# Kernel optimization log

Measured on AMD Instinct MI355X. Metric: run time of the kernel, lower is better.

Reference implementation:

```python
import jax, jax.numpy as jnp
import numpy as np

N = 100_000   # num destination nodes (adj rows)
M = 100_000   # num source/neighbor nodes (adj cols)
E = 3_200_000 # num edges (avg degree 32)
D_IN = 128
DIM = 128
LEAKY_ALPHA = 0.2  # tf.nn.leaky_relu default


def setup_inputs() -> dict:
    key = jax.random.key(0)
    ks = jax.random.split(key, 7)
    return {
        "self_embedding": jax.random.normal(ks[0], (N, D_IN), jnp.float32),
        "neigh_embedding": jax.random.normal(ks[1], (M, D_IN), jnp.float32),
        "W": jax.random.normal(ks[2], (D_IN, DIM), jnp.float32) / np.sqrt(D_IN).astype(np.float32),
        "w_self": jax.random.normal(ks[3], (DIM, 1), jnp.float32) * 0.1,
        "w_neigh": jax.random.normal(ks[4], (DIM, 1), jnp.float32) * 0.1,
        "edge_row": jax.random.randint(ks[5], (E,), 0, N, jnp.int32),
        "edge_col": jax.random.randint(ks[6], (E,), 0, M, jnp.int32),
    }


def reference(self_embedding, neigh_embedding, W, w_self, w_neigh, edge_row, edge_col):
    # Dense projections (shared weight, no bias)
    from_all = neigh_embedding @ W    # [M, DIM]
    from_self = self_embedding @ W    # [N, DIM]

    # Per-node attention logits
    self_weight = (from_self @ w_self)[:, 0]   # [N]
    all_weight = (from_all @ w_neigh)[:, 0]    # [M]

    # Per-edge score: leaky_relu(self_weight[row] + all_weight[col])
    scores = jax.nn.leaky_relu(self_weight[edge_row] + all_weight[edge_col],
                               negative_slope=LEAKY_ALPHA)  # [E]

    n = self_embedding.shape[0]
    # Sparse (segment) softmax over each row's edges, numerically stable
    row_max = jax.ops.segment_max(scores, edge_row, num_segments=n)
    row_max = jnp.where(jnp.isfinite(row_max), row_max, 0.0)  # guard empty rows
    e = jnp.exp(scores - row_max[edge_row])
    denom = jax.ops.segment_sum(e, edge_row, num_segments=n)
    denom = jnp.where(denom > 0, denom, 1.0)
    alpha = e / denom[edge_row]  # [E]

    # Sparse-dense matmul: output[i] = sum_j alpha_ij * from_all[j]
    agg = jax.ops.segment_sum(alpha[:, None] * from_all[edge_col], edge_row,
                              num_segments=n)  # [N, DIM]

    # renorm=False path: residual with from_self, then activation
    return jax.nn.relu(from_self + agg)
```

## Files before the change

### kernel.cpp

```cpp
#include <hip/hip_runtime.h>
#include <math.h>

#define DIM 128
#define LEAKY 0.2f
#define CAP 80
#define RPB 128
#define NBMAX 1024
#define PART_CHUNK 4096

typedef __attribute__((ext_vector_type(8))) short short8_t;
typedef __attribute__((ext_vector_type(8))) __bf16 bf16x8;
typedef __attribute__((ext_vector_type(4))) float f32x4;

__device__ __forceinline__ unsigned short f32_to_bf16_bits(float x) {
  unsigned u = __float_as_uint(x);
  u += 0x7fffu + ((u >> 16) & 1u);
  return (unsigned short)(u >> 16);
}

template <typename OT>
__global__ __launch_bounds__(256) void gemm_proj_mfma(
    const float* __restrict__ emb, const float* __restrict__ W,
    const float* __restrict__ wvec, OT* __restrict__ out,
    float* __restrict__ wout, int nrows)
{
  __shared__ unsigned short Wt[128 * 136];
  int t = threadIdx.x;
  int lane = t & 63;
  int wid = t >> 6;

  for (int i = t; i < 4096; i += 256) {
    int k = i >> 5;
    int c4 = (i & 31) << 2;
    float4 w4 = *(const float4*)(W + k * 128 + c4);
    Wt[(c4 + 0) * 136 + k] = f32_to_bf16_bits(w4.x);
    Wt[(c4 + 1) * 136 + k] = f32_to_bf16_bits(w4.y);
    Wt[(c4 + 2) * 136 + k] = f32_to_bf16_bits(w4.z);
    Wt[(c4 + 3) * 136 + k] = f32_to_bf16_bits(w4.w);
  }
  __syncthreads();

  int row0 = blockIdx.x * 128 + wid * 32;
  if (row0 >= nrows) return;

  int lr = lane & 15;
  int lk = lane >> 4;

  bf16x8 a[2][4];
#pragma unroll
  for (int rf = 0; rf < 2; rf++) {
    int row = row0 + rf * 16 + lr;
    row = min(row, nrows - 1);
    const float* src = emb + (size_t)row * DIM;
#pragma unroll
    for (int ks = 0; ks < 4; ks++) {
      int kb = ks * 32 + lk * 8;
      float4 x = *(const float4*)(src + kb);
      float4 y = *(const float4*)(src + kb + 4);
      union { short8_t s; bf16x8 b; } f;
      f.s[0] = (short)f32_to_bf16_bits(x.x); f.s[1] = (short)f32_to_bf16_bits(x.y);
      f.s[2] = (short)f32_to_bf16_bits(x.z); f.s[3] = (short)f32_to_bf16_bits(x.w);
      f.s[4] = (short)f32_to_bf16_bits(y.x); f.s[5] = (short)f32_to_bf16_bits(y.y);
      f.s[6] = (short)f32_to_bf16_bits(y.z); f.s[7] = (short)f32_to_bf16_bits(y.w);
      a[rf][ks] = f.b;
    }
  }

  f32x4 acc[2][8];
#pragma unroll
  for (int rf = 0; rf < 2; rf++)
#pragma unroll
    for (int cf = 0; cf < 8; cf++)
      acc[rf][cf] = (f32x4){0.f, 0.f, 0.f, 0.f};

#pragma unroll
  for (int ks = 0; ks < 4; ks++) {
#pragma unroll
    for (int cf = 0; cf < 8; cf++) {
      bf16x8 wf = *(const bf16x8*)(Wt + (cf * 16 + lr) * 136 + ks * 32 + lk * 8);
      acc[0][cf] = __builtin_amdgcn_mfma_f32_16x16x32_bf16(a[0][ks], wf, acc[0][cf], 0, 0, 0);
      acc[1][cf] = __builtin_amdgcn_mfma_f32_16x16x32_bf16(a[1][ks], wf, acc[1][cf], 0, 0, 0);
    }
  }

#pragma unroll
  for (int rf = 0; rf < 2; rf++) {
    float pp[4] = {0.f, 0.f, 0.f, 0.f};
#pragma unroll
    for (int cf = 0; cf < 8; cf++) {
      float wvv = wvec[cf * 16 + lr];
#pragma unroll
      for (int r = 0; r < 4; r++) pp[r] += acc[rf][cf][r] * wvv;
    }
#pragma unroll
    for (int r = 0; r < 4; r++) {
      pp[r] += __shfl_xor(pp[r], 1);
      pp[r] += __shfl_xor(pp[r], 2);
      pp[r] += __shfl_xor(pp[r], 4);
      pp[r] += __shfl_xor(pp[r], 8);
    }
#pragma unroll
    for (int r = 0; r < 4; r++) {
      int row = row0 + rf * 16 + lk * 4 + r;
      if (row < nrows) {
        if (lr == 0) wout[row] = pp[r];
#pragma unroll
        for (int cf = 0; cf < 8; cf++) {
          int col = cf * 16 + lr;
          if constexpr (sizeof(OT) == 4)
            ((float*)out)[(size_t)row * DIM + col] = acc[rf][cf][r];
          else
            ((unsigned short*)out)[(size_t)row * DIM + col] = f32_to_bf16_bits(acc[rf][cf][r]);
        }
      }
    }
  }
}

__global__ __launch_bounds__(256) void quantize_rows(
    const unsigned short* __restrict__ fa_bf16,
    unsigned char* __restrict__ fa_i8, float* __restrict__ scales, int M)
{
  int wid = threadIdx.x >> 6;
  int lane = threadIdx.x & 63;
  int row = blockIdx.x * 4 + wid;
  if (row >= M) return;
  unsigned u = ((const unsigned*)(fa_bf16 + (size_t)row * DIM))[lane];
  float v0 = __uint_as_float(u << 16);
  float v1 = __uint_as_float(u & 0xffff0000u);
  float m = fmaxf(fabsf(v0), fabsf(v1));
#pragma unroll
  for (int off = 32; off >= 1; off >>= 1) m = fmaxf(m, __shfl_xor(m, off));
  float inv = m > 0.f ? 127.f / m : 0.f;
  int q0 = (int)__builtin_rintf(v0 * inv) + 128;
  int q1 = (int)__builtin_rintf(v1 * inv) + 128;
  ((unsigned short*)(fa_i8 + (size_t)row * DIM))[lane] =
      (unsigned short)((q0 & 0xff) | ((q1 & 0xff) << 8));
  if (lane == 0) scales[row] = m * (1.f / 127.f);
}

__global__ void zero_gcur(int* __restrict__ gcur, int nb)
{
  int i = blockIdx.x * blockDim.x + threadIdx.x;
  if (i < nb) gcur[i] = 0;
}

__global__ __launch_bounds__(256) void partition_edges(
    const int* __restrict__ erow, const int* __restrict__ ecol,
    unsigned* __restrict__ streams, int capB, int* __restrict__ gcur,
    int E, int nb)
{
  __shared__ int cnt[NBMAX];
  __shared__ int base_[NBMAX];
  __shared__ int pos[NBMAX];
  int t = threadIdx.x;
  for (int i = t; i < nb; i += 256) { cnt[i] = 0; pos[i] = 0; }
  __syncthreads();

  int e0 = blockIdx.x * PART_CHUNK + t * 16;
  int rows[16], cols[16];
#pragma unroll
  for (int q = 0; q < 4; q++) {
    int e = e0 + q * 4;
    if (e + 3 < E) {
      *(int4*)(rows + q * 4) = *(const int4*)(erow + e);
      *(int4*)(cols + q * 4) = *(const int4*)(ecol + e);
    } else {
#pragma unroll
      for (int j = 0; j < 4; j++) {
        rows[q * 4 + j] = (e + j < E) ? erow[e + j] : -1;
        cols[q * 4 + j] = (e + j < E) ? ecol[e + j] : 0;
      }
    }
  }
#pragma unroll
  for (int j = 0; j < 16; j++)
    if (rows[j] >= 0) atomicAdd(&cnt[rows[j] >> 7], 1);
  __syncthreads();
  for (int i = t; i < nb; i += 256)
    base_[i] = cnt[i] ? atomicAdd(gcur + i, cnt[i]) : 0;
  __syncthreads();
#pragma unroll
  for (int j = 0; j < 16; j++) {
    if (rows[j] >= 0) {
      int b = rows[j] >> 7;
      int idx = base_[b] + atomicAdd(&pos[b], 1);
      if (idx < capB)
        streams[(size_t)b * capB + idx] =
            (unsigned)cols[j] | ((unsigned)(rows[j] & (RPB - 1)) << 20);
    }
  }
}

__global__ __launch_bounds__(256) void bucket_scatter(
    const unsigned* __restrict__ streams, int capB,
    const int* __restrict__ gcur, int* __restrict__ perm,
    int* __restrict__ deg, int N)
{
  __shared__ __align__(16) unsigned slots[RPB * CAP];
  __shared__ int cnt[RPB];
  int b = blockIdx.x;
  int t = threadIdx.x;
  for (int i = t; i < RPB; i += 256) cnt[i] = 0;
  __syncthreads();

  int n = min(gcur[b], capB);
  const unsigned* s = streams + (size_t)b * capB;
  for (int i = t; i < n; i += 256) {
    unsigned v = s[i];
    int rl = v >> 20;
    int p = atomicAdd(&cnt[rl], 1);
    if (p < CAP) slots[rl * CAP + p] = v & 0xFFFFFu;
  }
  __syncthreads();

  int row0 = b * RPB;
  unsigned* dst = (unsigned*)(perm + (size_t)row0 * CAP);
  for (int i = t; i < RPB * CAP / 4; i += 256)
    *(uint4*)(dst + i * 4) = *(const uint4*)(slots + i * 4);
  for (int i = t; i < RPB; i += 256) {
    int row = row0 + i;
    if (row < N) deg[row] = min(cnt[i], CAP);
  }
}

__global__ __launch_bounds__(256) void aggregate_kernel(
    const unsigned char* __restrict__ fa_i8,
    const float* __restrict__ scales,
    const int* __restrict__ perm, const int* __restrict__ deg_arr,
    const float* __restrict__ sw, const float* __restrict__ aw,
    float* __restrict__ out, int n)
{
  int wid = threadIdx.x >> 6;
  int lane = threadIdx.x & 63;
  int row = blockIdx.x * 4 + wid;
  if (row >= n) return;
  int deg = deg_arr[row];
  size_t base = (size_t)row * CAP;

  int g  = lane >> 3;
  int sl = lane & 7;

  size_t o = (size_t)row * DIM + sl * 16;
  float4 rr0, rr1, rr2, rr3;
  if (g == 0) {
    rr0 = *(const float4*)(out + o);
    rr1 = *(const float4*)(out + o + 4);
    rr2 = *(const float4*)(out + o + 8);
    rr3 = *(const float4*)(out + o + 12);
  }

  float acc[16];
#pragma unroll
  for (int k = 0; k < 16; k++) acc[k] = 0.f;
  float dsum = 0.f, Bl = 0.f;
  float swr = sw[row];

  for (int bb = 0; bb < deg; bb += 64) {
    int nact = min(64, deg - bb);
    int c = 0; float e = 0.f, a = 0.f;
    if (lane < nact) {
      c = perm[base + bb + lane];
      float v = swr + aw[c];
      v = v > 0.f ? v : LEAKY * v;
      e = __expf(v);
      a = e * scales[c];
    }
    dsum += e;

    for (int half = 0; half < 2; half++) {
      if (half * 32 >= nact) break;
#pragma unroll
      for (int jj = 0; jj < 4; jj++) {
        int eidx = half * 32 + (jj << 3) + g;
        float aj = __shfl(a, eidx);
        int   cj = __shfl(c, eidx);
        uint4 u = *(const uint4*)(fa_i8 + (size_t)cj * DIM + sl * 16);
        Bl += aj;
        acc[0]  += aj * (float)( u.x        & 0xffu);
        acc[1]  += aj * (float)((u.x >> 8 ) & 0xffu);
        acc[2]  += aj * (float)((u.x >> 16) & 0xffu);
        acc[3]  += aj * (float)( u.x >> 24);
        acc[4]  += aj * (float)( u.y        & 0xffu);
        acc[5]  += aj * (float)((u.y >> 8 ) & 0xffu);
        acc[6]  += aj * (float)((u.y >> 16) & 0xffu);
        acc[7]  += aj * (float)( u.y >> 24);
        acc[8]  += aj * (float)( u.z        & 0xffu);
        acc[9]  += aj * (float)((u.z >> 8 ) & 0xffu);
        acc[10] += aj * (float)((u.z >> 16) & 0xffu);
        acc[11] += aj * (float)( u.z >> 24);
        acc[12] += aj * (float)( u.w        & 0xffu);
        acc[13] += aj * (float)((u.w >> 8 ) & 0xffu);
        acc[14] += aj * (float)((u.w >> 16) & 0xffu);
        acc[15] += aj * (float)( u.w >> 24);
      }
    }
  }

#pragma unroll
  for (int off = 32; off >= 1; off >>= 1) dsum += __shfl_xor(dsum, off);
  Bl += __shfl_xor(Bl, 8); Bl += __shfl_xor(Bl, 16); Bl += __shfl_xor(Bl, 32);
#pragma unroll
  for (int k = 0; k < 16; k++) {
    acc[k] += __shfl_xor(acc[k], 8);
    acc[k] += __shfl_xor(acc[k], 16);
    acc[k] += __shfl_xor(acc[k], 32);
  }
  float B = -128.f * Bl;
  float inv = dsum > 0.f ? 1.f / dsum : 1.f;

  if (g == 0) {
    float r[16] = {rr0.x, rr0.y, rr0.z, rr0.w, rr1.x, rr1.y, rr1.z, rr1.w,
                   rr2.x, rr2.y, rr2.z, rr2.w, rr3.x, rr3.y, rr3.z, rr3.w};
#pragma unroll
    for (int k = 0; k < 16; k++) {
      float x = r[k] + (acc[k] + B) * inv;
      r[k] = x > 0.f ? x : 0.f;
    }
    *(float4*)(out + o)      = make_float4(r[0],  r[1],  r[2],  r[3]);
    *(float4*)(out + o + 4)  = make_float4(r[4],  r[5],  r[6],  r[7]);
    *(float4*)(out + o + 8)  = make_float4(r[8],  r[9],  r[10], r[11]);
    *(float4*)(out + o + 12) = make_float4(r[12], r[13], r[14], r[15]);
  }
}

extern "C" void kernel_launch(void* const* d_in, const int* in_sizes, int n_in,
                              void* d_out, int out_size, void* d_ws, size_t ws_size,
                              hipStream_t stream)
{
  const float* self_emb  = (const float*)d_in[0];
  const float* neigh_emb = (const float*)d_in[1];
  const float* W         = (const float*)d_in[2];
  const float* w_self    = (const float*)d_in[3];
  const float* w_neigh   = (const float*)d_in[4];
  const int*   erow      = (const int*)d_in[5];
  const int*   ecol      = (const int*)d_in[6];

  const int N = in_sizes[0] / DIM;
  const int M = in_sizes[1] / DIM;
  const int E = in_sizes[5];

  float* out = (float*)d_out;

  char* ws = (char*)d_ws;
  size_t off = 0;
  auto alloc = [&](size_t bytes) -> char* {
    char* p = ws + off;
    off += (bytes + 255) & ~(size_t)255;
    return p;
  };
  unsigned short* from_all = (unsigned short*)alloc((size_t)M * DIM * sizeof(unsigned short));
  unsigned char*  fa_i8    = (unsigned char*)alloc((size_t)M * DIM);
  float* scales  = (float*)alloc((size_t)M * sizeof(float));
  float* all_w   = (float*)alloc((size_t)M * sizeof(float));
  float* self_w  = (float*)alloc((size_t)N * sizeof(float));
  int*   deg     = (int*)alloc((size_t)N * sizeof(int));
  int*   gcur    = (int*)alloc(NBMAX * sizeof(int));
  int*   perm    = (int*)alloc((size_t)N * CAP * sizeof(int));

  const int nb = (N + RPB - 1) / RPB;
  const int capB = E / nb + 1024;
  unsigned* streams = (unsigned*)alloc((size_t)nb * capB * sizeof(unsigned));

  gemm_proj_mfma<unsigned short><<<(M + 127) / 128, 256, 0, stream>>>(neigh_emb, W, w_neigh, from_all, all_w, M);
  quantize_rows<<<(M + 3) / 4, 256, 0, stream>>>(from_all, fa_i8, scales, M);
  gemm_proj_mfma<float><<<(N + 127) / 128, 256, 0, stream>>>(self_emb, W, w_self, out, self_w, N);

  zero_gcur<<<(nb + 255) / 256, 256, 0, stream>>>(gcur, nb);

  int pblocks = (E + PART_CHUNK - 1) / PART_CHUNK;
  partition_edges<<<pblocks, 256, 0, stream>>>(erow, ecol, streams, capB, gcur, E, nb);

  bucket_scatter<<<nb, 256, 0, stream>>>(streams, capB, gcur, perm, deg, N);

  aggregate_kernel<<<(N + 3) / 4, 256, 0, stream>>>(fa_i8, scales, perm, deg,
                                                    self_w, all_w, out, N);
}
```

Baseline: 250.5 us.

## Merge independent preprocessing stages into two heterogeneous combo kernel launches

Edge partitioning and the neighbour projection GEMM now run as one launch, and bucket scatter, int8 quantization and the self projection GEMM run as a second launch. Each block picks its role from its block index, and shared memory is sized to the largest role. The aim is to cut launch count and let independent work fill the GPU at the same time, while raising shared memory use for the lighter roles. The zeroing kernel is replaced by hipMemsetAsync, and the scatter writes only the perm slots it filled instead of whole CAP-wide rows.

Result: slower. 258.3 us (+3.1%).

```diff
diff --git a/kernel.cpp b/kernel.cpp
--- a/kernel.cpp
+++ b/kernel.cpp
@@ -19,12 +19,12 @@
 }
 
 template <typename OT>
-__global__ __launch_bounds__(256) void gemm_proj_mfma(
-    const float* __restrict__ emb, const float* __restrict__ W,
-    const float* __restrict__ wvec, OT* __restrict__ out,
-    float* __restrict__ wout, int nrows)
-{
-  __shared__ unsigned short Wt[128 * 136];
+__device__ __forceinline__ void gemm_body(
+    int bid, char* smem_, const float* __restrict__ emb,
+    const float* __restrict__ W, const float* __restrict__ wvec,
+    OT* __restrict__ out, float* __restrict__ wout, int nrows)
+{
+  unsigned short* Wt = (unsigned short*)smem_;
   int t = threadIdx.x;
   int lane = t & 63;
   int wid = t >> 6;
@@ -40,7 +40,7 @@
   }
   __syncthreads();
 
-  int row0 = blockIdx.x * 128 + wid * 32;
+  int row0 = bid * 128 + wid * 32;
   if (row0 >= nrows) return;
 
   int lr = lane & 15;
@@ -117,13 +117,95 @@
   }
 }
 
-__global__ __launch_bounds__(256) void quantize_rows(
-    const unsigned short* __restrict__ fa_bf16,
+__device__ __forceinline__ void partition_body(
+    int bid, char* smem_, const int* __restrict__ erow,
+    const int* __restrict__ ecol, unsigned* __restrict__ streams,
+    int capB, int* __restrict__ gcur, int E, int nb)
+{
+  int* cnt   = (int*)smem_;
+  int* base_ = cnt + NBMAX;
+  int* pos   = base_ + NBMAX;
+  int t = threadIdx.x;
+  for (int i = t; i < nb; i += 256) { cnt[i] = 0; pos[i] = 0; }
+  __syncthreads();
+
+  int e0 = bid * PART_CHUNK + t * 16;
+  int rows[16], cols[16];
+#pragma unroll
+  for (int q = 0; q < 4; q++) {
+    int e = e0 + q * 4;
+    if (e + 3 < E) {
+      *(int4*)(rows + q * 4) = *(const int4*)(erow + e);
+      *(int4*)(cols + q * 4) = *(const int4*)(ecol + e);
+    } else {
+#pragma unroll
+      for (int j = 0; j < 4; j++) {
+        rows[q * 4 + j] = (e + j < E) ? erow[e + j] : -1;
+        cols[q * 4 + j] = (e + j < E) ? ecol[e + j] : 0;
+      }
+    }
+  }
+#pragma unroll
+  for (int j = 0; j < 16; j++)
+    if (rows[j] >= 0) atomicAdd(&cnt[rows[j] >> 7], 1);
+  __syncthreads();
+  for (int i = t; i < nb; i += 256)
+    base_[i] = cnt[i] ? atomicAdd(gcur + i, cnt[i]) : 0;
+  __syncthreads();
+#pragma unroll
+  for (int j = 0; j < 16; j++) {
+    if (rows[j] >= 0) {
+      int b = rows[j] >> 7;
+      int idx = base_[b] + atomicAdd(&pos[b], 1);
+      if (idx < capB)
+        streams[(size_t)b * capB + idx] =
+            (unsigned)cols[j] | ((unsigned)(rows[j] & (RPB - 1)) << 20);
+    }
+  }
+}
+
+__device__ __forceinline__ void scatter_body(
+    int bid, char* smem_, const unsigned* __restrict__ streams, int capB,
+    const int* __restrict__ gcur, int* __restrict__ perm,
+    int* __restrict__ deg, int N)
+{
+  unsigned* slots = (unsigned*)smem_;
+  int* cnt = (int*)(smem_ + RPB * CAP * 4);
+  int t = threadIdx.x;
+  for (int i = t; i < RPB; i += 256) cnt[i] = 0;
+  __syncthreads();
+
+  int n = min(gcur[bid], capB);
+  const unsigned* s = streams + (size_t)bid * capB;
+  for (int i = t; i < n; i += 256) {
+    unsigned v = s[i];
+    int rl = v >> 20;
+    int p = atomicAdd(&cnt[rl], 1);
+    if (p < CAP) slots[rl * CAP + p] = v & 0xFFFFFu;
+  }
+  __syncthreads();
+
+  int row0 = bid * RPB;
+  unsigned* dst = (unsigned*)(perm + (size_t)row0 * CAP);
+  const int W4 = CAP / 4;
+  for (int i = t; i < RPB * W4; i += 256) {
+    int rl = i / W4, w = i - rl * W4;
+    if (w * 4 < min(cnt[rl], CAP))
+      *(uint4*)(dst + rl * CAP + w * 4) = *(const uint4*)(slots + rl * CAP + w * 4);
+  }
+  for (int i = t; i < RPB; i += 256) {
+    int row = row0 + i;
+    if (row < N) deg[row] = min(cnt[i], CAP);
+  }
+}
+
+__device__ __forceinline__ void quantize_body(
+    int bid, const unsigned short* __restrict__ fa_bf16,
     unsigned char* __restrict__ fa_i8, float* __restrict__ scales, int M)
 {
   int wid = threadIdx.x >> 6;
   int lane = threadIdx.x & 63;
-  int row = blockIdx.x * 4 + wid;
+  int row = bid * 4 + wid;
   if (row >= M) return;
   unsigned u = ((const unsigned*)(fa_bf16 + (size_t)row * DIM))[lane];
   float v0 = __uint_as_float(u << 16);
@@ -139,89 +221,38 @@
   if (lane == 0) scales[row] = m * (1.f / 127.f);
 }
 
-__global__ void zero_gcur(int* __restrict__ gcur, int nb)
-{
-  int i = blockIdx.x * blockDim.x + threadIdx.x;
-  if (i < nb) gcur[i] = 0;
-}
-
-__global__ __launch_bounds__(256) void partition_edges(
-    const int* __restrict__ erow, const int* __restrict__ ecol,
-    unsigned* __restrict__ streams, int capB, int* __restrict__ gcur,
-    int E, int nb)
-{
-  __shared__ int cnt[NBMAX];
-  __shared__ int base_[NBMAX];
-  __shared__ int pos[NBMAX];
-  int t = threadIdx.x;
-  for (int i = t; i < nb; i += 256) { cnt[i] = 0; pos[i] = 0; }
-  __syncthreads();
-
-  int e0 = blockIdx.x * PART_CHUNK + t * 16;
-  int rows[16], cols[16];
-#pragma unroll
-  for (int q = 0; q < 4; q++) {
-    int e = e0 + q * 4;
-    if (e + 3 < E) {
-      *(int4*)(rows + q * 4) = *(const int4*)(erow + e);
-      *(int4*)(cols + q * 4) = *(const int4*)(ecol + e);
-    } else {
-#pragma unroll
-      for (int j = 0; j < 4; j++) {
-        rows[q * 4 + j] = (e + j < E) ? erow[e + j] : -1;
-        cols[q * 4 + j] = (e + j < E) ? ecol[e + j] : 0;
-      }
-    }
-  }
-#pragma unroll
-  for (int j = 0; j < 16; j++)
-    if (rows[j] >= 0) atomicAdd(&cnt[rows[j] >> 7], 1);
-  __syncthreads();
-  for (int i = t; i < nb; i += 256)
-    base_[i] = cnt[i] ? atomicAdd(gcur + i, cnt[i]) : 0;
-  __syncthreads();
-#pragma unroll
-  for (int j = 0; j < 16; j++) {
-    if (rows[j] >= 0) {
-      int b = rows[j] >> 7;
-      int idx = base_[b] + atomicAdd(&pos[b], 1);
-      if (idx < capB)
-        streams[(size_t)b * capB + idx] =
-            (unsigned)cols[j] | ((unsigned)(rows[j] & (RPB - 1)) << 20);
-    }
-  }
-}
-
-__global__ __launch_bounds__(256) void bucket_scatter(
-    const unsigned* __restrict__ streams, int capB,
-    const int* __restrict__ gcur, int* __restrict__ perm,
-    int* __restrict__ deg, int N)
-{
-  __shared__ __align__(16) unsigned slots[RPB * CAP];
-  __shared__ int cnt[RPB];
+__global__ __launch_bounds__(256) void combo1_kernel(
+    const int* erow, const int* ecol, unsigned* streams, int capB,
+    int* gcur, int E, int nb, int nPart,
+    const float* neigh_emb, const float* W, const float* w_neigh,
+    unsigned short* from_all, float* all_w, int M)
+{
+  __shared__ __align__(16) char smem[34816];
   int b = blockIdx.x;
-  int t = threadIdx.x;
-  for (int i = t; i < RPB; i += 256) cnt[i] = 0;
-  __syncthreads();
-
-  int n = min(gcur[b], capB);
-  const unsigned* s = streams + (size_t)b * capB;
-  for (int i = t; i < n; i += 256) {
-    unsigned v = s[i];
-    int rl = v >> 20;
-    int p = atomicAdd(&cnt[rl], 1);
-    if (p < CAP) slots[rl * CAP + p] = v & 0xFFFFFu;
-  }
-  __syncthreads();
-
-  int row0 = b * RPB;
-  unsigned* dst = (unsigned*)(perm + (size_t)row0 * CAP);
-  for (int i = t; i < RPB * CAP / 4; i += 256)
-    *(uint4*)(dst + i * 4) = *(const uint4*)(slots + i * 4);
-  for (int i = t; i < RPB; i += 256) {
-    int row = row0 + i;
-    if (row < N) deg[row] = min(cnt[i], CAP);
-  }
+  if (b < nPart)
+    partition_body(b, smem, erow, ecol, streams, capB, gcur, E, nb);
+  else
+    gemm_body<unsigned short>(b - nPart, smem, neigh_emb, W, w_neigh,
+                              from_all, all_w, M);
+}
+
+__global__ __launch_bounds__(256) void combo2_kernel(
+    const unsigned* streams, int capB, const int* gcur, int* perm,
+    int* deg, int N, int nScat,
+    const unsigned short* from_all, unsigned char* fa_i8, float* scales,
+    int M, int nQuant,
+    const float* self_emb, const float* W, const float* w_self,
+    float* out, float* self_w)
+{
+  __shared__ __align__(16) char smem[41472];
+  int b = blockIdx.x;
+  if (b < nScat)
+    scatter_body(b, smem, streams, capB, gcur, perm, deg, N);
+  else if (b < nScat + nQuant)
+    quantize_body(b - nScat, from_all, fa_i8, scales, M);
+  else
+    gemm_body<float>(b - nScat - nQuant, smem, self_emb, W, w_self,
+                     out, self_w, N);
 }
 
 __global__ __launch_bounds__(256) void aggregate_kernel(
@@ -362,16 +393,21 @@
   const int capB = E / nb + 1024;
   unsigned* streams = (unsigned*)alloc((size_t)nb * capB * sizeof(unsigned));
 
-  gemm_proj_mfma<unsigned short><<<(M + 127) / 128, 256, 0, stream>>>(neigh_emb, W, w_neigh, from_all, all_w, M);
-  quantize_rows<<<(M + 3) / 4, 256, 0, stream>>>(from_all, fa_i8, scales, M);
-  gemm_proj_mfma<float><<<(N + 127) / 128, 256, 0, stream>>>(self_emb, W, w_self, out, self_w, N);
-
-  zero_gcur<<<(nb + 255) / 256, 256, 0, stream>>>(gcur, nb);
-
-  int pblocks = (E + PART_CHUNK - 1) / PART_CHUNK;
-  partition_edges<<<pblocks, 256, 0, stream>>>(erow, ecol, streams, capB, gcur, E, nb);
-
-  bucket_scatter<<<nb, 256, 0, stream>>>(streams, capB, gcur, perm, deg, N);
+  const int nPart  = (E + PART_CHUNK - 1) / PART_CHUNK;
+  const int gblkM  = (M + 127) / 128;
+  const int gblkN  = (N + 127) / 128;
+  const int nQuant = (M + 3) / 4;
+
+  hipMemsetAsync(gcur, 0, nb * sizeof(int), stream);
+
+  combo1_kernel<<<nPart + gblkM, 256, 0, stream>>>(
+      erow, ecol, streams, capB, gcur, E, nb, nPart,
+      neigh_emb, W, w_neigh, from_all, all_w, M);
+
+  combo2_kernel<<<nb + nQuant + gblkN, 256, 0, stream>>>(
+      streams, capB, gcur, perm, deg, N, nb,
+      from_all, fa_i8, scales, M, nQuant,
+      self_emb, W, w_self, out, self_w);
 
   aggregate_kernel<<<(N + 3) / 4, 256, 0, stream>>>(fa_i8, scales, perm, deg,
                                                     self_w, all_w, out, N);
```

## Fuse int8 quantization into neighbor GEMM and merge bucket scatter with aggregation

Applied to the files above, without the earlier changes.

The neighbor projection GEMM now computes per-row absmax and writes int8 rows plus scales directly via an LDS staging buffer, eliminating the bf16 intermediate and the separate quantize kernel. Bucket scatter and aggregation are merged so each block aggregates its 128 rows straight from the LDS slot lists, removing the perm/deg global round trip. The zero kernel is replaced by a memset. The trade-off is far fewer, LDS-heavy blocks for the gather-bound aggregation phase, reducing occupancy and parallelism for latency hiding.

Result: slower. 284.5 us (+13.6%).

```diff
diff --git a/kernel.cpp b/kernel.cpp
--- a/kernel.cpp
+++ b/kernel.cpp
@@ -18,10 +18,133 @@
   return (unsigned short)(u >> 16);
 }
 
-template <typename OT>
-__global__ __launch_bounds__(256) void gemm_proj_mfma(
+__global__ __launch_bounds__(256) void gemm_neigh_q(
     const float* __restrict__ emb, const float* __restrict__ W,
-    const float* __restrict__ wvec, OT* __restrict__ out,
+    const float* __restrict__ wvec, unsigned char* __restrict__ fa_i8,
+    float* __restrict__ scales, float* __restrict__ wout, int nrows)
+{
+  __shared__ __align__(16) char smem[34816];
+  unsigned short* Wt = (unsigned short*)smem;
+  int t = threadIdx.x;
+  int lane = t & 63;
+  int wid = t >> 6;
+
+  for (int i = t; i < 4096; i += 256) {
+    int k = i >> 5;
+    int c4 = (i & 31) << 2;
+    float4 w4 = *(const float4*)(W + k * 128 + c4);
+    Wt[(c4 + 0) * 136 + k] = f32_to_bf16_bits(w4.x);
+    Wt[(c4 + 1) * 136 + k] = f32_to_bf16_bits(w4.y);
+    Wt[(c4 + 2) * 136 + k] = f32_to_bf16_bits(w4.z);
+    Wt[(c4 + 3) * 136 + k] = f32_to_bf16_bits(w4.w);
+  }
+  __syncthreads();
+
+  int row0 = blockIdx.x * 128 + wid * 32;
+  bool active = row0 < nrows;
+  int lr = lane & 15;
+  int lk = lane >> 4;
+
+  f32x4 acc[2][8];
+  if (active) {
+    bf16x8 a[2][4];
+#pragma unroll
+    for (int rf = 0; rf < 2; rf++) {
+      int row = row0 + rf * 16 + lr;
+      row = min(row, nrows - 1);
+      const float* src = emb + (size_t)row * DIM;
+#pragma unroll
+      for (int ks = 0; ks < 4; ks++) {
+        int kb = ks * 32 + lk * 8;
+        float4 x = *(const float4*)(src + kb);
+        float4 y = *(const float4*)(src + kb + 4);
+        union { short8_t s; bf16x8 b; } f;
+        f.s[0] = (short)f32_to_bf16_bits(x.x); f.s[1] = (short)f32_to_bf16_bits(x.y);
+        f.s[2] = (short)f32_to_bf16_bits(x.z); f.s[3] = (short)f32_to_bf16_bits(x.w);
+        f.s[4] = (short)f32_to_bf16_bits(y.x); f.s[5] = (short)f32_to_bf16_bits(y.y);
+        f.s[6] = (short)f32_to_bf16_bits(y.z); f.s[7] = (short)f32_to_bf16_bits(y.w);
+        a[rf][ks] = f.b;
+      }
+    }
+#pragma unroll
+    for (int rf = 0; rf < 2; rf++)
+#pragma unroll
+      for (int cf = 0; cf < 8; cf++)
+        acc[rf][cf] = (f32x4){0.f, 0.f, 0.f, 0.f};
+#pragma unroll
+    for (int ks = 0; ks < 4; ks++) {
+#pragma unroll
+      for (int cf = 0; cf < 8; cf++) {
+        bf16x8 wf = *(const bf16x8*)(Wt + (cf * 16 + lr) * 136 + ks * 32 + lk * 8);
+        acc[0][cf] = __builtin_amdgcn_mfma_f32_16x16x32_bf16(a[0][ks], wf, acc[0][cf], 0, 0, 0);
+        acc[1][cf] = __builtin_amdgcn_mfma_f32_16x16x32_bf16(a[1][ks], wf, acc[1][cf], 0, 0, 0);
+      }
+    }
+  }
+  __syncthreads();
+
+  unsigned char* Q = (unsigned char*)smem + wid * 4096;
+  if (active) {
+#pragma unroll
+    for (int rf = 0; rf < 2; rf++) {
+      float pp[4] = {0.f, 0.f, 0.f, 0.f};
+#pragma unroll
+      for (int cf = 0; cf < 8; cf++) {
+        float wvv = wvec[cf * 16 + lr];
+#pragma unroll
+        for (int r = 0; r < 4; r++) pp[r] += acc[rf][cf][r] * wvv;
+      }
+#pragma unroll
+      for (int r = 0; r < 4; r++) {
+        pp[r] += __shfl_xor(pp[r], 1);
+        pp[r] += __shfl_xor(pp[r], 2);
+        pp[r] += __shfl_xor(pp[r], 4);
+        pp[r] += __shfl_xor(pp[r], 8);
+      }
+      float m[4];
+#pragma unroll
+      for (int r = 0; r < 4; r++) {
+        float mm = 0.f;
+#pragma unroll
+        for (int cf = 0; cf < 8; cf++) mm = fmaxf(mm, fabsf(acc[rf][cf][r]));
+        mm = fmaxf(mm, __shfl_xor(mm, 1));
+        mm = fmaxf(mm, __shfl_xor(mm, 2));
+        mm = fmaxf(mm, __shfl_xor(mm, 4));
+        mm = fmaxf(mm, __shfl_xor(mm, 8));
+        m[r] = mm;
+      }
+#pragma unroll
+      for (int r = 0; r < 4; r++) {
+        int rl = rf * 16 + lk * 4 + r;
+        int row = row0 + rl;
+        float inv = m[r] > 0.f ? 127.f / m[r] : 0.f;
+        if (row < nrows && lr == 0) {
+          wout[row] = pp[r];
+          scales[row] = m[r] * (1.f / 127.f);
+        }
+#pragma unroll
+        for (int cf = 0; cf < 8; cf++) {
+          int q = (int)__builtin_rintf(acc[rf][cf][r] * inv) + 128;
+          Q[rl * 128 + cf * 16 + lr] = (unsigned char)(q & 0xff);
+        }
+      }
+    }
+  }
+  __syncthreads();
+
+  if (active) {
+    unsigned char* dstb = fa_i8 + (size_t)row0 * DIM;
+    int nbytes = min(32, nrows - row0) * DIM;
+    for (int i = lane * 16; i < 4096; i += 1024) {
+      if (i < nbytes)
+        *(uint4*)(dstb + i) = *(const uint4*)(Q + i);
+    }
+  }
+}
+
+__global__ __launch_bounds__(256) void gemm_self_f32(
+    const float* __restrict__ emb, const float* __restrict__ W,
+    const float* __restrict__ wvec, float* __restrict__ out,
     float* __restrict__ wout, int nrows)
 {
   __shared__ unsigned short Wt[128 * 136];
@@ -105,44 +228,11 @@
       if (row < nrows) {
         if (lr == 0) wout[row] = pp[r];
 #pragma unroll
-        for (int cf = 0; cf < 8; cf++) {
-          int col = cf * 16 + lr;
-          if constexpr (sizeof(OT) == 4)
-            ((float*)out)[(size_t)row * DIM + col] = acc[rf][cf][r];
-          else
-            ((unsigned short*)out)[(size_t)row * DIM + col] = f32_to_bf16_bits(acc[rf][cf][r]);
-        }
-      }
-    }
-  }
-}
-
-__global__ __launch_bounds__(256) void quantize_rows(
-    const unsigned short* __restrict__ fa_bf16,
-    unsigned char* __restrict__ fa_i8, float* __restrict__ scales, int M)
-{
-  int wid = threadIdx.x >> 6;
-  int lane = threadIdx.x & 63;
-  int row = blockIdx.x * 4 + wid;
-  if (row >= M) return;
-  unsigned u = ((const unsigned*)(fa_bf16 + (size_t)row * DIM))[lane];
-  float v0 = __uint_as_float(u << 16);
-  float v1 = __uint_as_float(u & 0xffff0000u);
-  float m = fmaxf(fabsf(v0), fabsf(v1));
-#pragma unroll
-  for (int off = 32; off >= 1; off >>= 1) m = fmaxf(m, __shfl_xor(m, off));
-  float inv = m > 0.f ? 127.f / m : 0.f;
-  int q0 = (int)__builtin_rintf(v0 * inv) + 128;
-  int q1 = (int)__builtin_rintf(v1 * inv) + 128;
-  ((unsigned short*)(fa_i8 + (size_t)row * DIM))[lane] =
-      (unsigned short)((q0 & 0xff) | ((q1 & 0xff) << 8));
-  if (lane == 0) scales[row] = m * (1.f / 127.f);
-}
-
-__global__ void zero_gcur(int* __restrict__ gcur, int nb)
-{
-  int i = blockIdx.x * blockDim.x + threadIdx.x;
-  if (i < nb) gcur[i] = 0;
+        for (int cf = 0; cf < 8; cf++)
+          out[(size_t)row * DIM + cf * 16 + lr] = acc[rf][cf][r];
+      }
+    }
+  }
 }
 
 __global__ __launch_bounds__(256) void partition_edges(
@@ -192,10 +282,12 @@
   }
 }
 
-__global__ __launch_bounds__(256) void bucket_scatter(
+__global__ __launch_bounds__(256) void scatter_aggregate(
     const unsigned* __restrict__ streams, int capB,
-    const int* __restrict__ gcur, int* __restrict__ perm,
-    int* __restrict__ deg, int N)
+    const int* __restrict__ gcur,
+    const unsigned char* __restrict__ fa_i8, const float* __restrict__ scales,
+    const float* __restrict__ sw, const float* __restrict__ aw,
+    float* __restrict__ out, int N)
 {
   __shared__ __align__(16) unsigned slots[RPB * CAP];
   __shared__ int cnt[RPB];
@@ -214,113 +306,98 @@
   }
   __syncthreads();
 
-  int row0 = b * RPB;
-  unsigned* dst = (unsigned*)(perm + (size_t)row0 * CAP);
-  for (int i = t; i < RPB * CAP / 4; i += 256)
-    *(uint4*)(dst + i * 4) = *(const uint4*)(slots + i * 4);
-  for (int i = t; i < RPB; i += 256) {
-    int row = row0 + i;
-    if (row < N) deg[row] = min(cnt[i], CAP);
-  }
-}
-
-__global__ __launch_bounds__(256) void aggregate_kernel(
-    const unsigned char* __restrict__ fa_i8,
-    const float* __restrict__ scales,
-    const int* __restrict__ perm, const int* __restrict__ deg_arr,
-    const float* __restrict__ sw, const float* __restrict__ aw,
-    float* __restrict__ out, int n)
-{
-  int wid = threadIdx.x >> 6;
-  int lane = threadIdx.x & 63;
-  int row = blockIdx.x * 4 + wid;
-  if (row >= n) return;
-  int deg = deg_arr[row];
-  size_t base = (size_t)row * CAP;
-
+  int wid = t >> 6;
+  int lane = t & 63;
   int g  = lane >> 3;
   int sl = lane & 7;
-
-  size_t o = (size_t)row * DIM + sl * 16;
-  float4 rr0, rr1, rr2, rr3;
-  if (g == 0) {
-    rr0 = *(const float4*)(out + o);
-    rr1 = *(const float4*)(out + o + 4);
-    rr2 = *(const float4*)(out + o + 8);
-    rr3 = *(const float4*)(out + o + 12);
-  }
-
-  float acc[16];
-#pragma unroll
-  for (int k = 0; k < 16; k++) acc[k] = 0.f;
-  float dsum = 0.f, Bl = 0.f;
-  float swr = sw[row];
-
-  for (int bb = 0; bb < deg; bb += 64) {
-    int nact = min(64, deg - bb);
-    int c = 0; float e = 0.f, a = 0.f;
-    if (lane < nact) {
-      c = perm[base + bb + lane];
-      float v = swr + aw[c];
-      v = v > 0.f ? v : LEAKY * v;
-      e = __expf(v);
-      a = e * scales[c];
-    }
-    dsum += e;
-
-    for (int half = 0; half < 2; half++) {
-      if (half * 32 >= nact) break;
-#pragma unroll
-      for (int jj = 0; jj < 4; jj++) {
-        int eidx = half * 32 + (jj << 3) + g;
-        float aj = __shfl(a, eidx);
-        int   cj = __shfl(c, eidx);
-        uint4 u = *(const uint4*)(fa_i8 + (size_t)cj * DIM + sl * 16);
-        Bl += aj;
-        acc[0]  += aj * (float)( u.x        & 0xffu);
-        acc[1]  += aj * (float)((u.x >> 8 ) & 0xffu);
-        acc[2]  += aj * (float)((u.x >> 16) & 0xffu);
-        acc[3]  += aj * (float)( u.x >> 24);
-        acc[4]  += aj * (float)( u.y        & 0xffu);
-        acc[5]  += aj * (float)((u.y >> 8 ) & 0xffu);
-        acc[6]  += aj * (float)((u.y >> 16) & 0xffu);
-        acc[7]  += aj * (float)( u.y >> 24);
-        acc[8]  += aj * (float)( u.z        & 0xffu);
-        acc[9]  += aj * (float)((u.z >> 8 ) & 0xffu);
-        acc[10] += aj * (float)((u.z >> 16) & 0xffu);
-        acc[11] += aj * (float)( u.z >> 24);
-        acc[12] += aj * (float)( u.w        & 0xffu);
-        acc[13] += aj * (float)((u.w >> 8 ) & 0xffu);
-        acc[14] += aj * (float)((u.w >> 16) & 0xffu);
-        acc[15] += aj * (float)( u.w >> 24);
-      }
-    }
-  }
-
-#pragma unroll
-  for (int off = 32; off >= 1; off >>= 1) dsum += __shfl_xor(dsum, off);
-  Bl += __shfl_xor(Bl, 8); Bl += __shfl_xor(Bl, 16); Bl += __shfl_xor(Bl, 32);
-#pragma unroll
-  for (int k = 0; k < 16; k++) {
-    acc[k] += __shfl_xor(acc[k], 8);
-    acc[k] += __shfl_xor(acc[k], 16);
-    acc[k] += __shfl_xor(acc[k], 32);
-  }
-  float B = -128.f * Bl;
-  float inv = dsum > 0.f ? 1.f / dsum : 1.f;
-
-  if (g == 0) {
-    float r[16] = {rr0.x, rr0.y, rr0.z, rr0.w, rr1.x, rr1.y, rr1.z, rr1.w,
-                   rr2.x, rr2.y, rr2.z, rr2.w, rr3.x, rr3.y, rr3.z, rr3.w};
+  int row0 = b * RPB;
+
+  for (int rl = wid; rl < RPB; rl += 4) {
+    int row = row0 + rl;
+    if (row >= N) break;
+    int deg = min(cnt[rl], CAP);
+    float swr = sw[row];
+
+    size_t o = (size_t)row * DIM + sl * 16;
+    float4 rr0, rr1, rr2, rr3;
+    if (g == 0) {
+      rr0 = *(const float4*)(out + o);
+      rr1 = *(const float4*)(out + o + 4);
+      rr2 = *(const float4*)(out + o + 8);
+      rr3 = *(const float4*)(out + o + 12);
+    }
+
+    float acc[16];
+#pragma unroll
+    for (int k = 0; k < 16; k++) acc[k] = 0.f;
+    float dsum = 0.f, Bl = 0.f;
+
+    for (int bb = 0; bb < deg; bb += 64) {
+      int nact = min(64, deg - bb);
+      int c = 0; float e = 0.f, a2 = 0.f;
+      if (lane < nact) {
+        c = (int)slots[rl * CAP + bb + lane];
+        float v = swr + aw[c];
+        v = v > 0.f ? v : LEAKY * v;
+        e = __expf(v);
+        a2 = e * scales[c];
+      }
+      dsum += e;
+
+      for (int half = 0; half < 2; half++) {
+        if (half * 32 >= nact) break;
+#pragma unroll
+        for (int jj = 0; jj < 4; jj++) {
+          int eidx = half * 32 + (jj << 3) + g;
+          float aj = __shfl(a2, eidx);
+          int   cj = __shfl(c, eidx);
+          uint4 u = *(const uint4*)(fa_i8 + (size_t)cj * DIM + sl * 16);
+          Bl += aj;
+          acc[0]  += aj * (float)( u.x        & 0xffu);
+          acc[1]  += aj * (float)((u.x >> 8 ) & 0xffu);
+          acc[2]  += aj * (float)((u.x >> 16) & 0xffu);
+          acc[3]  += aj * (float)( u.x >> 24);
+          acc[4]  += aj * (float)( u.y        & 0xffu);
+          acc[5]  += aj * (float)((u.y >> 8 ) & 0xffu);
+          acc[6]  += aj * (float)((u.y >> 16) & 0xffu);
+          acc[7]  += aj * (float)( u.y >> 24);
+          acc[8]  += aj * (float)( u.z        & 0xffu);
+          acc[9]  += aj * (float)((u.z >> 8 ) & 0xffu);
+          acc[10] += aj * (float)((u.z >> 16) & 0xffu);
+          acc[11] += aj * (float)( u.z >> 24);
+          acc[12] += aj * (float)( u.w        & 0xffu);
+          acc[13] += aj * (float)((u.w >> 8 ) & 0xffu);
+          acc[14] += aj * (float)((u.w >> 16) & 0xffu);
+          acc[15] += aj * (float)( u.w >> 24);
+        }
+      }
+    }
+
+#pragma unroll
+    for (int off = 32; off >= 1; off >>= 1) dsum += __shfl_xor(dsum, off);
+    Bl += __shfl_xor(Bl, 8); Bl += __shfl_xor(Bl, 16); Bl += __shfl_xor(Bl, 32);
 #pragma unroll
     for (int k = 0; k < 16; k++) {
-      float x = r[k] + (acc[k] + B) * inv;
-      r[k] = x > 0.f ? x : 0.f;
-    }
-    *(float4*)(out + o)      = make_float4(r[0],  r[1],  r[2],  r[3]);
-    *(float4*)(out + o + 4)  = make_float4(r[4],  r[5],  r[6],  r[7]);
-    *(float4*)(out + o + 8)  = make_float4(r[8],  r[9],  r[10], r[11]);
-    *(float4*)(out + o + 12) = make_float4(r[12], r[13], r[14], r[15]);
+      acc[k] += __shfl_xor(acc[k], 8);
+      acc[k] += __shfl_xor(acc[k], 16);
+      acc[k] += __shfl_xor(acc[k], 32);
+    }
+    float B = -128.f * Bl;
+    float inv = dsum > 0.f ? 1.f / dsum : 1.f;
+
+    if (g == 0) {
+      float r[16] = {rr0.x, rr0.y, rr0.z, rr0.w, rr1.x, rr1.y, rr1.z, rr1.w,
+                     rr2.x, rr2.y, rr2.z, rr2.w, rr3.x, rr3.y, rr3.z, rr3.w};
+#pragma unroll
+      for (int k = 0; k < 16; k++) {
+        float x = r[k] + (acc[k] + B) * inv;
+        r[k] = x > 0.f ? x : 0.f;
+      }
+      *(float4*)(out + o)      = make_float4(r[0],  r[1],  r[2],  r[3]);
+      *(float4*)(out + o + 4)  = make_float4(r[4],  r[5],  r[6],  r[7]);
+      *(float4*)(out + o + 8)  = make_float4(r[8],  r[9],  r[10], r[11]);
+      *(float4*)(out + o + 12) = make_float4(r[12], r[13], r[14], r[15]);
+    }
   }
 }
 
@@ -349,30 +426,27 @@
     off += (bytes + 255) & ~(size_t)255;
     return p;
   };
-  unsigned short* from_all = (unsigned short*)alloc((size_t)M * DIM * sizeof(unsigned short));
-  unsigned char*  fa_i8    = (unsigned char*)alloc((size_t)M * DIM);
-  float* scales  = (float*)alloc((size_t)M * sizeof(float));
-  float* all_w   = (float*)alloc((size_t)M * sizeof(float));
-  float* self_w  = (float*)alloc((size_t)N * sizeof(float));
-  int*   deg     = (int*)alloc((size_t)N * sizeof(int));
-  int*   gcur    = (int*)alloc(NBMAX * sizeof(int));
-  int*   perm    = (int*)alloc((size_t)N * CAP * sizeof(int));
+  unsigned char* fa_i8  = (unsigned char*)alloc((size_t)M * DIM);
+  float* scales = (float*)alloc((size_t)M * sizeof(float));
+  float* all_w  = (float*)alloc((size_t)M * sizeof(float));
+  float* self_w = (float*)alloc((size_t)N * sizeof(float));
+  int*   gcur   = (int*)alloc(NBMAX * sizeof(int));
 
   const int nb = (N + RPB - 1) / RPB;
   const int capB = E / nb + 1024;
   unsigned* streams = (unsigned*)alloc((size_t)nb * capB * sizeof(unsigned));
 
-  gemm_proj_mfma<unsigned short><<<(M + 127) / 128, 256, 0, stream>>>(neigh_emb, W, w_neigh, from_all, all_w, M);
-  quantize_rows<<<(M + 3) / 4, 256, 0, stream>>>(from_all, fa_i8, scales, M);
-  gemm_proj_mfma<float><<<(N + 127) / 128, 256, 0, stream>>>(self_emb, W, w_self, out, self_w, N);
-
-  zero_gcur<<<(nb + 255) / 256, 256, 0, stream>>>(gcur, nb);
+  hipMemsetAsync(gcur, 0, nb * sizeof(int), stream);
+
+  gemm_neigh_q<<<(M + 127) / 128, 256, 0, stream>>>(neigh_emb, W, w_neigh,
+                                                    fa_i8, scales, all_w, M);
+
+  gemm_self_f32<<<(N + 127) / 128, 256, 0, stream>>>(self_emb, W, w_self,
+                                                     out, self_w, N);
 
   int pblocks = (E + PART_CHUNK - 1) / PART_CHUNK;
   partition_edges<<<pblocks, 256, 0, stream>>>(erow, ecol, streams, capB, gcur, E, nb);
 
-  bucket_scatter<<<nb, 256, 0, stream>>>(streams, capB, gcur, perm, deg, N);
-
-  aggregate_kernel<<<(N + 3) / 4, 256, 0, stream>>>(fa_i8, scales, perm, deg,
-                                                    self_w, all_w, out, N);
-}
+  scatter_aggregate<<<nb, 256, 0, stream>>>(streams, capB, gcur, fa_i8, scales,
+                                            self_w, all_w, out, N);
+}
```
